# Optimization experiments

Measured on AMD Instinct MI355X. Metric: run time of the kernel, lower is better.

## Reference

```python
import jax, jax.numpy as jnp
import numpy as np

EMB = 1024
HEADS = 16
HEAD_DIM = EMB // HEADS
SEQ = 2048
BATCH = 2
FF = 4 * EMB


def gelu_tanh(x):
    # matches the hand-rolled GELU: 0.5*x*(1+tanh(sqrt(2/pi)*(x+0.044715*x^3)))
    c = jnp.sqrt(jnp.asarray(2.0 / jnp.pi, dtype=x.dtype))
    return 0.5 * x * (1.0 + jnp.tanh(c * (x + 0.044715 * x ** 3)))


def layernorm(x, scale, shift, eps=1e-5):
    mean = jnp.mean(x, axis=-1, keepdims=True)
    var = jnp.var(x, axis=-1, keepdims=True)  # unbiased=False
    return scale * (x - mean) * jax.lax.rsqrt(var + eps) + shift


def setup_inputs() -> dict:
    key = jax.random.key(0)
    ks = jax.random.split(key, 10)
    s = 1.0 / np.sqrt(EMB)
    sf = 1.0 / np.sqrt(FF)
    return {
        "x": jax.random.normal(ks[0], (BATCH, SEQ, EMB), jnp.float32),
        "Wq": jax.random.uniform(ks[1], (EMB, EMB), jnp.float32, -s, s),
        "Wk": jax.random.uniform(ks[2], (EMB, EMB), jnp.float32, -s, s),
        "Wv": jax.random.uniform(ks[3], (EMB, EMB), jnp.float32, -s, s),
        "Wo": jax.random.uniform(ks[4], (EMB, EMB), jnp.float32, -s, s),
        "bo": jnp.zeros((EMB,), jnp.float32),
        "ln1_g": jnp.ones((EMB,), jnp.float32),
        "ln1_b": jnp.zeros((EMB,), jnp.float32),
        "ln2_g": jnp.ones((EMB,), jnp.float32),
        "ln2_b": jnp.zeros((EMB,), jnp.float32),
        "W1": jax.random.uniform(ks[5], (EMB, FF), jnp.float32, -s, s),
        "b1": jnp.zeros((FF,), jnp.float32),
        "W2": jax.random.uniform(ks[6], (FF, EMB), jnp.float32, -sf, sf),
        "b2": jnp.zeros((EMB,), jnp.float32),
    }


def reference(x, Wq, Wk, Wv, Wo, bo, ln1_g, ln1_b, ln2_g, ln2_b, W1, b1, W2, b2):
    b, n, d = x.shape
    shortcut = x
    h = layernorm(x, ln1_g, ln1_b)
    # projections -> [b, heads, n, head_dim]
    def split_heads(t):
        return t.reshape(b, n, HEADS, HEAD_DIM).transpose(0, 2, 1, 3)
    q = split_heads(h @ Wq)
    k = split_heads(h @ Wk)
    v = split_heads(h @ Wv)
    scores = jnp.einsum("bhqd,bhkd->bhqk", q, k)
    causal = jnp.triu(jnp.ones((n, n), dtype=bool), k=1)
    scores = jnp.where(causal, -jnp.inf, scores)
    weights = jax.nn.softmax(scores / jnp.sqrt(jnp.asarray(HEAD_DIM, x.dtype)), axis=-1)
    ctx = jnp.einsum("bhqk,bhkd->bhqd", weights, v)
    ctx = ctx.transpose(0, 2, 1, 3).reshape(b, n, d)
    attn_out = ctx @ Wo + bo
    x = attn_out + shortcut
    shortcut = x
    h = layernorm(x, ln2_g, ln2_b)
    ff = gelu_tanh(h @ W1 + b1) @ W2 + b2
    return ff + shortcut
```

## Files before the change

kernel.cpp:

```cpp
#include <hip/hip_runtime.h>

typedef __bf16 bf16x8 __attribute__((ext_vector_type(8)));
typedef float f32x4 __attribute__((ext_vector_type(4)));
typedef unsigned short u16;

#define EMB 1024
#define SEQ 2048
#define BATCH 2
#define HEADS 16
#define HEAD_DIM 64
#define FF 4096
#define ROWS (BATCH * SEQ)

static __device__ __forceinline__ u16 f2bf(float f) {
    unsigned int u = __builtin_bit_cast(unsigned int, f);
    unsigned int r = (u + 0x7FFFu + ((u >> 16) & 1u)) >> 16;
    return (u16)r;
}

__global__ __launch_bounds__(256) void transpose_f32_to_bf16(
    const float* __restrict__ in, u16* __restrict__ out, int R, int C) {
    __shared__ float tile[32][33];
    int c0 = blockIdx.x * 32, r0 = blockIdx.y * 32;
    int tx = threadIdx.x & 31, ty = threadIdx.x >> 5;
#pragma unroll
    for (int i = 0; i < 32; i += 8)
        tile[ty + i][tx] = in[(size_t)(r0 + ty + i) * C + c0 + tx];
    __syncthreads();
#pragma unroll
    for (int i = 0; i < 32; i += 8)
        out[(size_t)(c0 + ty + i) * R + r0 + tx] = f2bf(tile[tx][ty + i]);
}

__global__ __launch_bounds__(256) void ln_kernel(
    const float* __restrict__ x, const float* __restrict__ gamma,
    const float* __restrict__ beta, u16* __restrict__ out) {
    int row = blockIdx.x;
    int t = threadIdx.x;
    float4 v = reinterpret_cast<const float4*>(x + (size_t)row * EMB)[t];
    float s = v.x + v.y + v.z + v.w;
    float s2 = v.x * v.x + v.y * v.y + v.z * v.z + v.w * v.w;
#pragma unroll
    for (int off = 1; off < 64; off <<= 1) {
        s += __shfl_xor(s, off);
        s2 += __shfl_xor(s2, off);
    }
    __shared__ float sm[8];
    int wid = t >> 6;
    if ((t & 63) == 0) { sm[wid] = s; sm[wid + 4] = s2; }
    __syncthreads();
    s = sm[0] + sm[1] + sm[2] + sm[3];
    s2 = sm[4] + sm[5] + sm[6] + sm[7];
    float mean = s * (1.0f / EMB);
    float var = s2 * (1.0f / EMB) - mean * mean;
    float inv = rsqrtf(var + 1e-5f);
    float4 gv = reinterpret_cast<const float4*>(gamma)[t];
    float4 bv = reinterpret_cast<const float4*>(beta)[t];
    ushort4 o;
    o.x = f2bf((v.x - mean) * inv * gv.x + bv.x);
    o.y = f2bf((v.y - mean) * inv * gv.y + bv.y);
    o.z = f2bf((v.z - mean) * inv * gv.z + bv.z);
    o.w = f2bf((v.w - mean) * inv * gv.w + bv.w);
    reinterpret_cast<ushort4*>(out + (size_t)row * EMB)[t] = o;
}

template <int EPI>
__global__ __launch_bounds__(256) void gemm_bf16(
    const u16* __restrict__ A, const u16* __restrict__ B, void* __restrict__ Cout,
    const float* __restrict__ bias, const float* __restrict__ resid,
    int M, int N, int K) {
    __shared__ u16 As[128 * 72];
    __shared__ u16 Bs[128 * 72];
    int tm = blockIdx.x * 128;
    int tn = blockIdx.y * 128;
    int t = threadIdx.x;
    int lane = t & 63, wid = t >> 6;
    int wr = (wid >> 1) * 64, wc = (wid & 1) * 64;
    int l15 = lane & 15, g = lane >> 4;
    f32x4 acc[4][4] = {};
    for (int k0 = 0; k0 < K; k0 += 64) {
        __syncthreads();
#pragma unroll
        for (int p = 0; p < 4; ++p) {
            int chunk = t + p * 256;
            int row = chunk >> 3, c16 = chunk & 7;
            uint4 av = *reinterpret_cast<const uint4*>(A + (size_t)(tm + row) * K + k0 + c16 * 8);
            *reinterpret_cast<uint4*>(&As[row * 72 + c16 * 8]) = av;
            uint4 bv = *reinterpret_cast<const uint4*>(B + (size_t)(tn + row) * K + k0 + c16 * 8);
            *reinterpret_cast<uint4*>(&Bs[row * 72 + c16 * 8]) = bv;
        }
        __syncthreads();
#pragma unroll
        for (int kc = 0; kc < 2; ++kc) {
            int ko = kc * 32 + g * 8;
            bf16x8 af[4], bfr[4];
#pragma unroll
            for (int i = 0; i < 4; ++i)
                af[i] = *reinterpret_cast<const bf16x8*>(&As[(wr + i * 16 + l15) * 72 + ko]);
#pragma unroll
            for (int j = 0; j < 4; ++j)
                bfr[j] = *reinterpret_cast<const bf16x8*>(&Bs[(wc + j * 16 + l15) * 72 + ko]);
#pragma unroll
            for (int i = 0; i < 4; ++i)
#pragma unroll
                for (int j = 0; j < 4; ++j)
                    acc[i][j] = __builtin_amdgcn_mfma_f32_16x16x32_bf16(af[i], bfr[j], acc[i][j], 0, 0, 0);
        }
    }
    int mb = tm + wr + g * 4;
    int nb = tn + wc + l15;
#pragma unroll
    for (int i = 0; i < 4; ++i) {
#pragma unroll
        for (int j = 0; j < 4; ++j) {
            int n = nb + j * 16;
#pragma unroll
            for (int r = 0; r < 4; ++r) {
                int m = mb + i * 16 + r;
                float val = acc[i][j][r];
                if constexpr (EPI == 0) {
                    ((u16*)Cout)[(size_t)m * N + n] = f2bf(val);
                } else if constexpr (EPI == 1) {
                    ((float*)Cout)[(size_t)m * N + n] =
                        val + bias[n] + resid[(size_t)m * N + n];
                } else if constexpr (EPI == 2) {
                    float xg = val + bias[n];
                    float x3 = xg + 0.044715f * xg * xg * xg;
                    float tz = 0.7978845608028654f * x3;
                    float th = 1.0f - 2.0f / (1.0f + __expf(2.0f * tz));
                    ((u16*)Cout)[(size_t)m * N + n] = f2bf(0.5f * xg * (1.0f + th));
                } else {
                    int bb = m >> 11, ss = m & 2047;
                    ((u16*)Cout)[((size_t)(bb * EMB + n)) * SEQ + ss] = f2bf(val);
                }
            }
        }
    }
}

__global__ __launch_bounds__(256) void attn_kernel(
    const u16* __restrict__ Qb, const u16* __restrict__ Kb,
    const u16* __restrict__ Vt, u16* __restrict__ ctx) {
    __shared__ u16 P_lds[4][32][72];
    int bh = blockIdx.x;
    int b = bh >> 4, h = bh & 15;
    int qtile = blockIdx.y;
    int lane = threadIdx.x & 63, wid = threadIdx.x >> 6;
    int l15 = lane & 15, g = lane >> 4;
    int qbase = qtile * 128 + wid * 32;

    bf16x8 qf[2][2];
#pragma unroll
    for (int qt = 0; qt < 2; ++qt)
#pragma unroll
        for (int kc = 0; kc < 2; ++kc)
            qf[qt][kc] = *reinterpret_cast<const bf16x8*>(
                Qb + (size_t)(b * SEQ + qbase + qt * 16 + l15) * EMB + h * 64 + kc * 32 + g * 8);

    f32x4 ctx_acc[2][4] = {};
    float mrun[2] = {-1e30f, -1e30f};
    float lrun[2] = {0.f, 0.f};
    int nkt = qbase / 64 + 1;

    for (int kt = 0; kt < nkt; ++kt) {
        int k0 = kt * 64;
        f32x4 sacc[4][2] = {};
#pragma unroll
        for (int kc = 0; kc < 2; ++kc) {
#pragma unroll
            for (int ktile = 0; ktile < 4; ++ktile) {
                bf16x8 kf = *reinterpret_cast<const bf16x8*>(
                    Kb + (size_t)(b * SEQ + k0 + ktile * 16 + l15) * EMB + h * 64 + kc * 32 + g * 8);
#pragma unroll
                for (int qt = 0; qt < 2; ++qt)
                    sacc[ktile][qt] = __builtin_amdgcn_mfma_f32_16x16x32_bf16(
                        kf, qf[qt][kc], sacc[ktile][qt], 0, 0, 0);
            }
        }
#pragma unroll
        for (int qt = 0; qt < 2; ++qt) {
            int q = qbase + qt * 16 + l15;
            float sv[16];
            float tmax = -1e30f;
#pragma unroll
            for (int ktile = 0; ktile < 4; ++ktile)
#pragma unroll
                for (int r = 0; r < 4; ++r) {
                    int key = k0 + ktile * 16 + g * 4 + r;
                    float sx = sacc[ktile][qt][r] * 0.125f;
                    if (key > q) sx = -1e30f;
                    sv[ktile * 4 + r] = sx;
                    tmax = fmaxf(tmax, sx);
                }
            tmax = fmaxf(tmax, __shfl_xor(tmax, 16));
            tmax = fmaxf(tmax, __shfl_xor(tmax, 32));
            float mnew = fmaxf(mrun[qt], tmax);
            float corr = __expf(mrun[qt] - mnew);
            mrun[qt] = mnew;
            float psum = 0.f;
#pragma unroll
            for (int idx = 0; idx < 16; ++idx) {
                float p = __expf(sv[idx] - mnew);
                sv[idx] = p;
                psum += p;
            }
            lrun[qt] = lrun[qt] * corr + psum;
            float corr4[4];
#pragma unroll
            for (int r = 0; r < 4; ++r) corr4[r] = __shfl(corr, g * 4 + r);
#pragma unroll
            for (int dt = 0; dt < 4; ++dt)
#pragma unroll
                for (int r = 0; r < 4; ++r) ctx_acc[qt][dt][r] *= corr4[r];
#pragma unroll
            for (int ktile = 0; ktile < 4; ++ktile)
#pragma unroll
                for (int r = 0; r < 4; ++r)
                    P_lds[wid][qt * 16 + l15][ktile * 16 + g * 4 + r] = f2bf(sv[ktile * 4 + r]);
        }
        asm volatile("s_waitcnt lgkmcnt(0)" ::: "memory");
#pragma unroll
        for (int kc = 0; kc < 2; ++kc) {
            bf16x8 pf[2];
#pragma unroll
            for (int qt = 0; qt < 2; ++qt)
                pf[qt] = *reinterpret_cast<const bf16x8*>(&P_lds[wid][qt * 16 + l15][kc * 32 + g * 8]);
#pragma unroll
            for (int dt = 0; dt < 4; ++dt) {
                bf16x8 vf = *reinterpret_cast<const bf16x8*>(
                    Vt + (size_t)(b * EMB + h * 64 + dt * 16 + l15) * SEQ + k0 + kc * 32 + g * 8);
#pragma unroll
                for (int qt = 0; qt < 2; ++qt)
                    ctx_acc[qt][dt] = __builtin_amdgcn_mfma_f32_16x16x32_bf16(
                        pf[qt], vf, ctx_acc[qt][dt], 0, 0, 0);
            }
        }
    }
#pragma unroll
    for (int qt = 0; qt < 2; ++qt) {
        float lsum = lrun[qt];
        lsum += __shfl_xor(lsum, 16);
        lsum += __shfl_xor(lsum, 32);
        float d4[4];
#pragma unroll
        for (int r = 0; r < 4; ++r) d4[r] = __shfl(lsum, g * 4 + r);
#pragma unroll
        for (int dt = 0; dt < 4; ++dt)
#pragma unroll
            for (int r = 0; r < 4; ++r) {
                int q = qbase + qt * 16 + g * 4 + r;
                int d = h * 64 + dt * 16 + l15;
                ctx[(size_t)(b * SEQ + q) * EMB + d] = f2bf(ctx_acc[qt][dt][r] / d4[r]);
            }
    }
}

extern "C" void kernel_launch(void* const* d_in, const int* in_sizes, int n_in,
                              void* d_out, int out_size, void* d_ws, size_t ws_size,
                              hipStream_t stream) {
    const float* x    = (const float*)d_in[0];
    const float* Wq   = (const float*)d_in[1];
    const float* Wk   = (const float*)d_in[2];
    const float* Wv   = (const float*)d_in[3];
    const float* Wo   = (const float*)d_in[4];
    const float* bo   = (const float*)d_in[5];
    const float* ln1g = (const float*)d_in[6];
    const float* ln1b = (const float*)d_in[7];
    const float* ln2g = (const float*)d_in[8];
    const float* ln2b = (const float*)d_in[9];
    const float* W1   = (const float*)d_in[10];
    const float* b1   = (const float*)d_in[11];
    const float* W2   = (const float*)d_in[12];
    const float* b2   = (const float*)d_in[13];

    char* ws = (char*)d_ws;
    size_t off = 0;
    auto alloc = [&](size_t bytes) {
        void* p = ws + off;
        off += (bytes + 255) & ~(size_t)255;
        return p;
    };
    u16* h1   = (u16*)alloc((size_t)ROWS * EMB * 2);
    u16* Wqt  = (u16*)alloc((size_t)EMB * EMB * 2);
    u16* Wkt  = (u16*)alloc((size_t)EMB * EMB * 2);
    u16* Wvt  = (u16*)alloc((size_t)EMB * EMB * 2);
    u16* Wot  = (u16*)alloc((size_t)EMB * EMB * 2);
    u16* W1t  = (u16*)alloc((size_t)FF * EMB * 2);
    u16* W2t  = (u16*)alloc((size_t)EMB * FF * 2);
    u16* Qb   = (u16*)alloc((size_t)ROWS * EMB * 2);
    u16* Kb   = (u16*)alloc((size_t)ROWS * EMB * 2);
    u16* Vtb  = (u16*)alloc((size_t)BATCH * EMB * SEQ * 2);
    u16* ctxb = (u16*)alloc((size_t)ROWS * EMB * 2);
    float* x2 = (float*)alloc((size_t)ROWS * EMB * 4);
    u16* h2   = (u16*)alloc((size_t)ROWS * EMB * 2);
    u16* ff1  = (u16*)alloc((size_t)ROWS * FF * 2);

    transpose_f32_to_bf16<<<dim3(32, 32), 256, 0, stream>>>(Wq, Wqt, EMB, EMB);
    transpose_f32_to_bf16<<<dim3(32, 32), 256, 0, stream>>>(Wk, Wkt, EMB, EMB);
    transpose_f32_to_bf16<<<dim3(32, 32), 256, 0, stream>>>(Wv, Wvt, EMB, EMB);
    transpose_f32_to_bf16<<<dim3(32, 32), 256, 0, stream>>>(Wo, Wot, EMB, EMB);
    transpose_f32_to_bf16<<<dim3(128, 32), 256, 0, stream>>>(W1, W1t, EMB, FF);
    transpose_f32_to_bf16<<<dim3(32, 128), 256, 0, stream>>>(W2, W2t, FF, EMB);

    ln_kernel<<<ROWS, 256, 0, stream>>>(x, ln1g, ln1b, h1);

    gemm_bf16<0><<<dim3(32, 8), 256, 0, stream>>>(h1, Wqt, Qb, nullptr, nullptr, ROWS, EMB, EMB);
    gemm_bf16<0><<<dim3(32, 8), 256, 0, stream>>>(h1, Wkt, Kb, nullptr, nullptr, ROWS, EMB, EMB);
    gemm_bf16<3><<<dim3(32, 8), 256, 0, stream>>>(h1, Wvt, Vtb, nullptr, nullptr, ROWS, EMB, EMB);

    attn_kernel<<<dim3(32, 16), 256, 0, stream>>>(Qb, Kb, Vtb, ctxb);

    gemm_bf16<1><<<dim3(32, 8), 256, 0, stream>>>(ctxb, Wot, x2, bo, x, ROWS, EMB, EMB);

    ln_kernel<<<ROWS, 256, 0, stream>>>(x2, ln2g, ln2b, h2);

    gemm_bf16<2><<<dim3(32, 32), 256, 0, stream>>>(h2, W1t, ff1, b1, nullptr, ROWS, FF, EMB);
    gemm_bf16<1><<<dim3(32, 8), 256, 0, stream>>>(ff1, W2t, (float*)d_out, b2, x2, ROWS, EMB, FF);
}
```

Baseline: 466.2 us.

## Fuse QKV GEMM, use direct global-to-LDS loads, and shrink attention blocks

Concatenates the transposed Wq/Wk/Wv into one weight buffer and runs a single N=3072 GEMM whose epilogue routes columns to Q, K, or transposed V. The GEMM staging now uses global_load_lds direct-to-LDS copies with an unpadded 64-wide tile, which drops the register round-trip but may add LDS bank conflicts on the fragment reads. Attention becomes one wave per block with 32 query rows, with the heaviest (last) query chunks scheduled first for causal load balance. It also writes P to LDS as packed ushort4 stores.

Result: slower. 481.0 us (+3.2%).

```diff
diff --git a/kernel.cpp b/kernel.cpp
--- a/kernel.cpp
+++ b/kernel.cpp
@@ -16,6 +16,12 @@
     unsigned int u = __builtin_bit_cast(unsigned int, f);
     unsigned int r = (u + 0x7FFFu + ((u >> 16) & 1u)) >> 16;
     return (u16)r;
+}
+
+static __device__ __forceinline__ void gload16(const u16* g, u16* l) {
+    __builtin_amdgcn_global_load_lds(
+        (const __attribute__((address_space(1))) unsigned int*)(const void*)g,
+        (__attribute__((address_space(3))) unsigned int*)(void*)l, 16, 0, 0);
 }
 
 __global__ __launch_bounds__(256) void transpose_f32_to_bf16(
@@ -68,26 +74,27 @@
 __global__ __launch_bounds__(256) void gemm_bf16(
     const u16* __restrict__ A, const u16* __restrict__ B, void* __restrict__ Cout,
     const float* __restrict__ bias, const float* __restrict__ resid,
+    void* __restrict__ Cout2, void* __restrict__ Cout3,
     int M, int N, int K) {
-    __shared__ u16 As[128 * 72];
-    __shared__ u16 Bs[128 * 72];
+    __shared__ u16 As[128 * 64];
+    __shared__ u16 Bs[128 * 64];
     int tm = blockIdx.x * 128;
     int tn = blockIdx.y * 128;
     int t = threadIdx.x;
     int lane = t & 63, wid = t >> 6;
     int wr = (wid >> 1) * 64, wc = (wid & 1) * 64;
     int l15 = lane & 15, g = lane >> 4;
+    const u16* Abase = A + (size_t)tm * K;
+    const u16* Bbase = B + (size_t)tn * K;
     f32x4 acc[4][4] = {};
     for (int k0 = 0; k0 < K; k0 += 64) {
         __syncthreads();
 #pragma unroll
         for (int p = 0; p < 4; ++p) {
-            int chunk = t + p * 256;
-            int row = chunk >> 3, c16 = chunk & 7;
-            uint4 av = *reinterpret_cast<const uint4*>(A + (size_t)(tm + row) * K + k0 + c16 * 8);
-            *reinterpret_cast<uint4*>(&As[row * 72 + c16 * 8]) = av;
-            uint4 bv = *reinterpret_cast<const uint4*>(B + (size_t)(tn + row) * K + k0 + c16 * 8);
-            *reinterpret_cast<uint4*>(&Bs[row * 72 + c16 * 8]) = bv;
+            int chunk = (wid * 4 + p) * 64 + lane;
+            int row = chunk >> 3, c8 = (chunk & 7) * 8;
+            gload16(Abase + (size_t)row * K + k0 + c8, &As[(wid * 4 + p) * 512]);
+            gload16(Bbase + (size_t)row * K + k0 + c8, &Bs[(wid * 4 + p) * 512]);
         }
         __syncthreads();
 #pragma unroll
@@ -96,10 +103,10 @@
             bf16x8 af[4], bfr[4];
 #pragma unroll
             for (int i = 0; i < 4; ++i)
-                af[i] = *reinterpret_cast<const bf16x8*>(&As[(wr + i * 16 + l15) * 72 + ko]);
+                af[i] = *reinterpret_cast<const bf16x8*>(&As[(wr + i * 16 + l15) * 64 + ko]);
 #pragma unroll
             for (int j = 0; j < 4; ++j)
-                bfr[j] = *reinterpret_cast<const bf16x8*>(&Bs[(wc + j * 16 + l15) * 72 + ko]);
+                bfr[j] = *reinterpret_cast<const bf16x8*>(&Bs[(wc + j * 16 + l15) * 64 + ko]);
 #pragma unroll
             for (int i = 0; i < 4; ++i)
 #pragma unroll
@@ -130,24 +137,30 @@
                     float th = 1.0f - 2.0f / (1.0f + __expf(2.0f * tz));
                     ((u16*)Cout)[(size_t)m * N + n] = f2bf(0.5f * xg * (1.0f + th));
                 } else {
-                    int bb = m >> 11, ss = m & 2047;
-                    ((u16*)Cout)[((size_t)(bb * EMB + n)) * SEQ + ss] = f2bf(val);
+                    if (n < 1024) {
+                        ((u16*)Cout)[(size_t)m * 1024 + n] = f2bf(val);
+                    } else if (n < 2048) {
+                        ((u16*)Cout2)[(size_t)m * 1024 + (n - 1024)] = f2bf(val);
+                    } else {
+                        int bb = m >> 11, ss = m & 2047;
+                        ((u16*)Cout3)[((size_t)(bb * EMB + (n - 2048))) * SEQ + ss] = f2bf(val);
+                    }
                 }
             }
         }
     }
 }
 
-__global__ __launch_bounds__(256) void attn_kernel(
+__global__ __launch_bounds__(64) void attn_kernel(
     const u16* __restrict__ Qb, const u16* __restrict__ Kb,
     const u16* __restrict__ Vt, u16* __restrict__ ctx) {
-    __shared__ u16 P_lds[4][32][72];
+    __shared__ u16 P_lds[32][72];
     int bh = blockIdx.x;
     int b = bh >> 4, h = bh & 15;
-    int qtile = blockIdx.y;
-    int lane = threadIdx.x & 63, wid = threadIdx.x >> 6;
+    int qc = 63 - (int)blockIdx.y;
+    int lane = threadIdx.x;
     int l15 = lane & 15, g = lane >> 4;
-    int qbase = qtile * 128 + wid * 32;
+    int qbase = qc * 32;
 
     bf16x8 qf[2][2];
 #pragma unroll
@@ -160,7 +173,7 @@
     f32x4 ctx_acc[2][4] = {};
     float mrun[2] = {-1e30f, -1e30f};
     float lrun[2] = {0.f, 0.f};
-    int nkt = qbase / 64 + 1;
+    int nkt = qc / 2 + 1;
 
     for (int kt = 0; kt < nkt; ++kt) {
         int k0 = kt * 64;
@@ -213,10 +226,14 @@
 #pragma unroll
                 for (int r = 0; r < 4; ++r) ctx_acc[qt][dt][r] *= corr4[r];
 #pragma unroll
-            for (int ktile = 0; ktile < 4; ++ktile)
-#pragma unroll
-                for (int r = 0; r < 4; ++r)
-                    P_lds[wid][qt * 16 + l15][ktile * 16 + g * 4 + r] = f2bf(sv[ktile * 4 + r]);
+            for (int ktile = 0; ktile < 4; ++ktile) {
+                ushort4 pk;
+                pk.x = f2bf(sv[ktile * 4 + 0]);
+                pk.y = f2bf(sv[ktile * 4 + 1]);
+                pk.z = f2bf(sv[ktile * 4 + 2]);
+                pk.w = f2bf(sv[ktile * 4 + 3]);
+                *reinterpret_cast<ushort4*>(&P_lds[qt * 16 + l15][ktile * 16 + g * 4]) = pk;
+            }
         }
         asm volatile("s_waitcnt lgkmcnt(0)" ::: "memory");
 #pragma unroll
@@ -224,7 +241,7 @@
             bf16x8 pf[2];
 #pragma unroll
             for (int qt = 0; qt < 2; ++qt)
-                pf[qt] = *reinterpret_cast<const bf16x8*>(&P_lds[wid][qt * 16 + l15][kc * 32 + g * 8]);
+                pf[qt] = *reinterpret_cast<const bf16x8*>(&P_lds[qt * 16 + l15][kc * 32 + g * 8]);
 #pragma unroll
             for (int dt = 0; dt < 4; ++dt) {
                 bf16x8 vf = *reinterpret_cast<const bf16x8*>(
@@ -280,20 +297,22 @@
         off += (bytes + 255) & ~(size_t)255;
         return p;
     };
-    u16* h1   = (u16*)alloc((size_t)ROWS * EMB * 2);
-    u16* Wqt  = (u16*)alloc((size_t)EMB * EMB * 2);
-    u16* Wkt  = (u16*)alloc((size_t)EMB * EMB * 2);
-    u16* Wvt  = (u16*)alloc((size_t)EMB * EMB * 2);
-    u16* Wot  = (u16*)alloc((size_t)EMB * EMB * 2);
-    u16* W1t  = (u16*)alloc((size_t)FF * EMB * 2);
-    u16* W2t  = (u16*)alloc((size_t)EMB * FF * 2);
-    u16* Qb   = (u16*)alloc((size_t)ROWS * EMB * 2);
-    u16* Kb   = (u16*)alloc((size_t)ROWS * EMB * 2);
-    u16* Vtb  = (u16*)alloc((size_t)BATCH * EMB * SEQ * 2);
-    u16* ctxb = (u16*)alloc((size_t)ROWS * EMB * 2);
-    float* x2 = (float*)alloc((size_t)ROWS * EMB * 4);
-    u16* h2   = (u16*)alloc((size_t)ROWS * EMB * 2);
-    u16* ff1  = (u16*)alloc((size_t)ROWS * FF * 2);
+    u16* h1     = (u16*)alloc((size_t)ROWS * EMB * 2);
+    u16* Wqkvt  = (u16*)alloc((size_t)3 * EMB * EMB * 2);
+    u16* Wot    = (u16*)alloc((size_t)EMB * EMB * 2);
+    u16* W1t    = (u16*)alloc((size_t)FF * EMB * 2);
+    u16* W2t    = (u16*)alloc((size_t)EMB * FF * 2);
+    u16* Qb     = (u16*)alloc((size_t)ROWS * EMB * 2);
+    u16* Kb     = (u16*)alloc((size_t)ROWS * EMB * 2);
+    u16* Vtb    = (u16*)alloc((size_t)BATCH * EMB * SEQ * 2);
+    u16* ctxb   = (u16*)alloc((size_t)ROWS * EMB * 2);
+    float* x2   = (float*)alloc((size_t)ROWS * EMB * 4);
+    u16* h2     = (u16*)alloc((size_t)ROWS * EMB * 2);
+    u16* ff1    = (u16*)alloc((size_t)ROWS * FF * 2);
+
+    u16* Wqt = Wqkvt;
+    u16* Wkt = Wqkvt + (size_t)EMB * EMB;
+    u16* Wvt = Wqkvt + (size_t)2 * EMB * EMB;
 
     transpose_f32_to_bf16<<<dim3(32, 32), 256, 0, stream>>>(Wq, Wqt, EMB, EMB);
     transpose_f32_to_bf16<<<dim3(32, 32), 256, 0, stream>>>(Wk, Wkt, EMB, EMB);
@@ -304,16 +323,18 @@
 
     ln_kernel<<<ROWS, 256, 0, stream>>>(x, ln1g, ln1b, h1);
 
-    gemm_bf16<0><<<dim3(32, 8), 256, 0, stream>>>(h1, Wqt, Qb, nullptr, nullptr, ROWS, EMB, EMB);
-    gemm_bf16<0><<<dim3(32, 8), 256, 0, stream>>>(h1, Wkt, Kb, nullptr, nullptr, ROWS, EMB, EMB);
-    gemm_bf16<3><<<dim3(32, 8), 256, 0, stream>>>(h1, Wvt, Vtb, nullptr, nullptr, ROWS, EMB, EMB);
-
-    attn_kernel<<<dim3(32, 16), 256, 0, stream>>>(Qb, Kb, Vtb, ctxb);
-
-    gemm_bf16<1><<<dim3(32, 8), 256, 0, stream>>>(ctxb, Wot, x2, bo, x, ROWS, EMB, EMB);
+    gemm_bf16<4><<<dim3(32, 24), 256, 0, stream>>>(h1, Wqkvt, Qb, nullptr, nullptr,
+                                                   Kb, Vtb, ROWS, 3072, EMB);
+
+    attn_kernel<<<dim3(32, 64), 64, 0, stream>>>(Qb, Kb, Vtb, ctxb);
+
+    gemm_bf16<1><<<dim3(32, 8), 256, 0, stream>>>(ctxb, Wot, x2, bo, x,
+                                                  nullptr, nullptr, ROWS, EMB, EMB);
 
     ln_kernel<<<ROWS, 256, 0, stream>>>(x2, ln2g, ln2b, h2);
 
-    gemm_bf16<2><<<dim3(32, 32), 256, 0, stream>>>(h2, W1t, ff1, b1, nullptr, ROWS, FF, EMB);
-    gemm_bf16<1><<<dim3(32, 8), 256, 0, stream>>>(ff1, W2t, (float*)d_out, b2, x2, ROWS, EMB, FF);
-}
+    gemm_bf16<2><<<dim3(32, 32), 256, 0, stream>>>(h2, W1t, ff1, b1, nullptr,
+                                                   nullptr, nullptr, ROWS, FF, EMB);
+    gemm_bf16<1><<<dim3(32, 8), 256, 0, stream>>>(ff1, W2t, (float*)d_out, b2, x2,
+                                                  nullptr, nullptr, ROWS, EMB, FF);
+}
```
